# Kernel tuning notes

Measured on AMD Instinct MI355X. Metric: run time of the kernel, lower is better.

The kernel has to match this reference:

```python
import jax, jax.numpy as jnp
import numpy as np

N_NODES = 100000
N_EDGES = 1600000
HIDDEN = 64
EDGE_DIM = 16


def setup_inputs() -> dict:
    key = jax.random.key(0)
    ks = jax.random.split(key, 9)
    x = jax.random.normal(ks[0], (N_NODES, HIDDEN), dtype=jnp.float32)
    edge_index = jax.random.randint(ks[1], (2, N_EDGES), 0, N_NODES, dtype=jnp.int32)
    edge_attr = jax.random.normal(ks[2], (N_EDGES, EDGE_DIM), dtype=jnp.float32)
    s1 = 1.0 / np.sqrt(HIDDEN * 2 + EDGE_DIM)
    s2 = 1.0 / np.sqrt(HIDDEN)
    s3 = 1.0 / np.sqrt(HIDDEN * 2)
    W1 = jax.random.uniform(ks[3], (HIDDEN * 2 + EDGE_DIM, HIDDEN), jnp.float32, -s1, s1)
    b1 = jax.random.uniform(ks[4], (HIDDEN,), jnp.float32, -s1, s1)
    W2 = jax.random.uniform(ks[5], (HIDDEN, HIDDEN), jnp.float32, -s2, s2)
    b2 = jax.random.uniform(ks[6], (HIDDEN,), jnp.float32, -s2, s2)
    W3 = jax.random.uniform(ks[7], (HIDDEN * 2, HIDDEN), jnp.float32, -s3, s3)
    b3 = jax.random.uniform(ks[8], (HIDDEN,), jnp.float32, -s3, s3)
    return {"x": x, "edge_index": edge_index, "edge_attr": edge_attr,
            "W1": W1, "b1": b1, "W2": W2, "b2": b2, "W3": W3, "b3": b3}


def reference(x, edge_index, edge_attr, W1, b1, W2, b2, W3, b3):
    src, dst = edge_index[0], edge_index[1]
    # edge MLP: Linear -> SiLU -> Linear -> SiLU
    m_in = jnp.concatenate([x[src], x[dst], edge_attr], axis=-1)  # [E, 2H+Ed]
    h = jax.nn.silu(m_in @ W1 + b1)
    messages = jax.nn.silu(h @ W2 + b2)  # [E, H]
    # scatter-add aggregate onto destination nodes
    agg = jax.ops.segment_sum(messages, dst, num_segments=x.shape[0])  # [N, H]
    # node MLP: Linear -> SiLU
    node_in = jnp.concatenate([x, agg], axis=-1)  # [N, 2H]
    return jax.nn.silu(node_in @ W3 + b3)
```

## Files before the change

kernel.cpp:

```cpp
#include <hip/hip_runtime.h>
#include <hip/hip_bf16.h>

#define NE 1600000
#define NN 100000
#define H 64
#define ED 16
#define NT (NE / 64)
#define NB1 391
#define NNB 1563

#define KS  72
#define K3S 136
#define YS  68

typedef __attribute__((ext_vector_type(8))) short short8;
typedef __attribute__((ext_vector_type(4))) float floatx4;

__device__ __forceinline__ unsigned short f2bf(float f) {
    union { float f; unsigned u; } v; v.f = f;
    unsigned r = v.u + 0x7fff + ((v.u >> 16) & 1);
    return (unsigned short)(r >> 16);
}

__device__ __forceinline__ float bf2f(unsigned short u) {
    union { unsigned u; float f; } v; v.u = ((unsigned)u) << 16;
    return v.f;
}

__device__ __forceinline__ unsigned cvt_pk_bf16(float lo, float hi) {
    unsigned r;
    asm("v_cvt_pk_bf16_f32 %0, %1, %2" : "=v"(r) : "v"(lo), "v"(hi));
    return r;
}

__device__ __forceinline__ float silu(float x) {
    return x * __builtin_amdgcn_rcpf(1.0f + __expf(-x));
}

__global__ void prep_kernel(const float* __restrict__ x,
                            const float* __restrict__ W1,
                            const float* __restrict__ b1,
                            const float* __restrict__ W2,
                            const float* __restrict__ W3,
                            const int* __restrict__ ei,
                            unsigned short* __restrict__ xb,
                            unsigned short* __restrict__ W1abT,
                            unsigned short* __restrict__ W1cT,
                            unsigned short* __restrict__ W2T,
                            unsigned short* __restrict__ W3T,
                            int* __restrict__ cnt,
                            int* __restrict__ rank,
                            float4* __restrict__ aggv) {
    int tid = blockIdx.x * blockDim.x + threadIdx.x;
    int nt = gridDim.x * blockDim.x;
    const float4* xv = (const float4*)x;
    uint2* xbv = (uint2*)xb;
    for (int i = tid; i < NN * H / 4; i += nt) {
        float4 v = xv[i];
        uint2 o;
        o.x = cvt_pk_bf16(v.x, v.y);
        o.y = cvt_pk_bf16(v.z, v.w);
        xbv[i] = o;
    }
    {
        float4 z = {0.f, 0.f, 0.f, 0.f};
        for (int i = tid; i < NN * H / 4; i += nt) aggv[i] = z;
    }
    for (int i = tid; i < 128 * KS; i += nt) {
        int n = i / KS, k = i % KS;
        W1abT[i] = (k < 64) ? f2bf(W1[(size_t)((n < 64) ? k : 64 + k) * 64 + (n & 63)])
                            : (unsigned short)0;
    }
    for (int i = tid; i < 64 * 32; i += nt) {
        int n = i / 32, k = i % 32;
        unsigned short v = 0;
        if (k < 16) v = f2bf(W1[(size_t)(128 + k) * 64 + n]);
        else if (k == 16) v = f2bf(b1[n]);
        W1cT[i] = v;
    }
    for (int i = tid; i < 64 * KS; i += nt) {
        int n = i / KS, k = i % KS;
        W2T[i] = (k < 64) ? f2bf(W2[k * 64 + n]) : (unsigned short)0;
    }
    for (int i = tid; i < 64 * K3S; i += nt) {
        int n = i / K3S, k = i % K3S;
        W3T[i] = (k < 128) ? f2bf(W3[k * 64 + n]) : (unsigned short)0;
    }
    for (int e = tid; e < NE; e += nt) {
        rank[e] = atomicAdd(&cnt[ei[NE + e]], 1);
    }
}

__global__ void scan_block_kernel(const int* __restrict__ cnt,
                                  int* __restrict__ offs,
                                  int* __restrict__ bsums) {
    __shared__ int tmp[256];
    int b = blockIdx.x, i = threadIdx.x, idx = b * 256 + i;
    int v = (idx < NN) ? cnt[idx] : 0;
    tmp[i] = v;
    __syncthreads();
    #pragma unroll
    for (int off = 1; off < 256; off <<= 1) {
        int t2 = (i >= off) ? tmp[i - off] : 0;
        __syncthreads();
        tmp[i] += t2;
        __syncthreads();
    }
    if (idx < NN) offs[idx] = tmp[i] - v;
    if (i == 255) bsums[b] = tmp[255];
}

__global__ void scan_sums_kernel(int* __restrict__ bsums) {
    __shared__ int tmp[512];
    int i = threadIdx.x;
    int v = (i < NB1) ? bsums[i] : 0;
    tmp[i] = v;
    __syncthreads();
    #pragma unroll
    for (int off = 1; off < 512; off <<= 1) {
        int t2 = (i >= off) ? tmp[i - off] : 0;
        __syncthreads();
        tmp[i] += t2;
        __syncthreads();
    }
    if (i < NB1) bsums[i] = tmp[i] - v;
}

__global__ void scan_add_kernel(int* __restrict__ offs,
                                const int* __restrict__ bsums) {
    int b = blockIdx.x, idx = b * 256 + threadIdx.x;
    if (idx < NN) {
        offs[idx] += bsums[b];
    }
}

__global__ void scatter_kernel(const int* __restrict__ ei,
                               const int* __restrict__ offs,
                               const int* __restrict__ rank,
                               unsigned long long* __restrict__ sSDE) {
    int e = blockIdx.x * 256 + threadIdx.x;
    int src = ei[e], dst = ei[NE + e];
    int pos = offs[dst] + rank[e];
    unsigned long long v = (unsigned long long)src
                         | ((unsigned long long)dst << 17)
                         | ((unsigned long long)e << 34);
    sSDE[pos] = v;
}

__global__ __launch_bounds__(256) void y12_kernel(
    const unsigned short* __restrict__ xb,
    const unsigned short* __restrict__ W1abT,
    unsigned short* __restrict__ yc) {
    __shared__ unsigned short sW[128 * KS];
    int t = threadIdx.x;
    {
        const uint4* wv = (const uint4*)W1abT;
        uint4* sv = (uint4*)sW;
        for (int i = t; i < 128 * KS * 2 / 16; i += 256) sv[i] = wv[i];
    }
    __syncthreads();

    int lane = t & 63, w = t >> 6;
    int m = lane & 15, q = lane >> 4;
    int n0 = blockIdx.x * 64;
    int node = n0 + w * 16 + m;
    int nclamp = (node < NN) ? node : (NN - 1);

    floatx4 acc[8];
    #pragma unroll
    for (int i = 0; i < 8; i++) acc[i] = (floatx4){0.f, 0.f, 0.f, 0.f};
    #pragma unroll
    for (int kt = 0; kt < 2; kt++) {
        short8 bfr = *(const short8*)(xb + (size_t)nclamp * H + kt * 32 + q * 8);
        #pragma unroll
        for (int tt = 0; tt < 8; tt++) {
            short8 afr = *(const short8*)(sW + (tt * 16 + m) * KS + kt * 32 + q * 8);
            acc[tt] = __builtin_amdgcn_mfma_f32_16x16x32_bf16(afr, bfr, acc[tt], 0, 0, 0);
        }
    }
    if (node < NN) {
        #pragma unroll
        for (int tt = 0; tt < 8; tt++) {
            uint2 o;
            o.x = cvt_pk_bf16(acc[tt][0], acc[tt][1]);
            o.y = cvt_pk_bf16(acc[tt][2], acc[tt][3]);
            *(uint2*)(yc + (size_t)node * 128 + tt * 16 + q * 4) = o;
        }
    }
}

__global__ __launch_bounds__(256, 8) void edge_kernel(
    const unsigned short* __restrict__ yc,
    const float* __restrict__ ea,
    const unsigned long long* __restrict__ sSDE,
    const unsigned short* __restrict__ W1cT,
    const unsigned short* __restrict__ W2T,
    const float* __restrict__ b2,
    float* __restrict__ agg) {
    __shared__ float sWS[4][1088];
    __shared__ int sDst[64];

    int t = threadIdx.x;
    int lane = t & 63, w = t >> 6;
    int m = lane & 15, q = lane >> 4;
    int E = w * 16 + m;

    unsigned long long sde = sSDE[(size_t)blockIdx.x * 64 + E];
    int src = (int)(sde & 0x1FFFF);
    int dst = (int)((sde >> 17) & 0x1FFFF);
    int e   = (int)(sde >> 34);
    if (q == 0) sDst[E] = dst;

    union uf { unsigned u[4]; short8 s; };
    uf idA, idB;
    {
        unsigned val = (m & 1) ? 0x3F800000u : 0x00003F80u;
        int wsel = (m >> 1) & 3;
        bool gA = (q == (m >> 3));
        bool gB = (q == 2 + (m >> 3));
        #pragma unroll
        for (int i = 0; i < 4; i++) {
            idA.u[i] = (gA && wsel == i) ? val : 0u;
            idB.u[i] = (gB && wsel == i) ? val : 0u;
        }
    }

    short8 y1f0 = *(const short8*)(yc + (size_t)src * 128 + q * 8);
    short8 y1f1 = *(const short8*)(yc + (size_t)src * 128 + 32 + q * 8);
    short8 y2f0 = *(const short8*)(yc + (size_t)dst * 128 + 64 + q * 8);
    short8 y2f1 = *(const short8*)(yc + (size_t)dst * 128 + 96 + q * 8);

    short8 bf1 = {0, 0, 0, 0, 0, 0, 0, 0};
    if (q < 2) {
        const float4* p = (const float4*)(ea + (size_t)e * ED + q * 8);
        float4 v0 = p[0], v1 = p[1];
        union { unsigned u[4]; short8 s; } ub;
        ub.u[0] = cvt_pk_bf16(v0.x, v0.y);
        ub.u[1] = cvt_pk_bf16(v0.z, v0.w);
        ub.u[2] = cvt_pk_bf16(v1.x, v1.y);
        ub.u[3] = cvt_pk_bf16(v1.z, v1.w);
        bf1 = ub.s;
    } else if (q == 2) {
        bf1[0] = (short)0x3F80;
    }

    floatx4 acc[4];
    #pragma unroll
    for (int tt = 0; tt < 4; tt++) {
        short8 w1c = *(const short8*)(W1cT + (tt * 16 + m) * 32 + q * 8);
        floatx4 a = (floatx4){0.f, 0.f, 0.f, 0.f};
        a = __builtin_amdgcn_mfma_f32_16x16x32_bf16(w1c, bf1, a, 0, 0, 0);
        short8 idt = (tt & 1) ? idB.s : idA.s;
        a = __builtin_amdgcn_mfma_f32_16x16x32_bf16(idt, (tt >> 1) ? y1f1 : y1f0, a, 0, 0, 0);
        a = __builtin_amdgcn_mfma_f32_16x16x32_bf16(idt, (tt >> 1) ? y2f1 : y2f0, a, 0, 0, 0);
        acc[tt] = a;
    }

    unsigned short* sHw = (unsigned short*)sWS[w];
    #pragma unroll
    for (int tt = 0; tt < 4; tt++) {
        uint2 hp;
        hp.x = cvt_pk_bf16(silu(acc[tt][0]), silu(acc[tt][1]));
        hp.y = cvt_pk_bf16(silu(acc[tt][2]), silu(acc[tt][3]));
        *(uint2*)(sHw + m * KS + tt * 16 + q * 4) = hp;
    }

    floatx4 acc2[4];
    #pragma unroll
    for (int i = 0; i < 4; i++) acc2[i] = (floatx4){0.f, 0.f, 0.f, 0.f};
    #pragma unroll
    for (int kt = 0; kt < 2; kt++) {
        short8 hfr = *(const short8*)(sHw + m * KS + kt * 32 + q * 8);
        #pragma unroll
        for (int tt = 0; tt < 4; tt++) {
            short8 w2 = *(const short8*)(W2T + (tt * 16 + m) * KS + kt * 32 + q * 8);
            acc2[tt] = __builtin_amdgcn_mfma_f32_16x16x32_bf16(w2, hfr, acc2[tt], 0, 0, 0);
        }
    }

    float* sMw = sWS[w];
    #pragma unroll
    for (int tt = 0; tt < 4; tt++) {
        float4 bb = *(const float4*)(b2 + tt * 16 + q * 4);
        float4 mv;
        mv.x = silu(acc2[tt][0] + bb.x);
        mv.y = silu(acc2[tt][1] + bb.y);
        mv.z = silu(acc2[tt][2] + bb.z);
        mv.w = silu(acc2[tt][3] + bb.w);
        *(float4*)(sMw + m * YS + tt * 16 + q * 4) = mv;
    }

    {
        int c = lane;
        float s = 0.f;
        int cur = sDst[w * 16];
        #pragma unroll
        for (int r = 0; r < 16; r++) {
            int d = sDst[w * 16 + r];
            if (d != cur) {
                atomicAdd(&agg[(size_t)cur * H + c], s);
                s = 0.f;
                cur = d;
            }
            s += sMw[r * YS + c];
        }
        atomicAdd(&agg[(size_t)cur * H + c], s);
    }
}

__global__ __launch_bounds__(256) void node_kernel(
    const unsigned short* __restrict__ xb,
    const float* __restrict__ agg,
    const unsigned short* __restrict__ W3T,
    const float* __restrict__ b3,
    float* __restrict__ out) {
    __shared__ unsigned short sW3[64 * K3S];
    __shared__ unsigned short sA[64 * K3S];

    int t = threadIdx.x;
    int n0 = blockIdx.x * 64;

    {
        const uint4* wv = (const uint4*)W3T;
        uint4* sv = (uint4*)sW3;
        for (int i = t; i < 64 * K3S * 2 / 16; i += 256) sv[i] = wv[i];
    }
    {
        int nL = t >> 2, sub = t & 3;
        int node = n0 + nL;
        uint4* arow = (uint4*)(sA + nL * K3S);
        if (node < NN) {
            const uint4* xs = (const uint4*)(xb + (size_t)node * H);
            arow[sub * 2]     = xs[sub * 2];
            arow[sub * 2 + 1] = xs[sub * 2 + 1];
            const float4* av = (const float4*)(agg + (size_t)node * H);
            unsigned tmp[8];
            #pragma unroll
            for (int j = 0; j < 4; j++) {
                float4 v = av[sub * 4 + j];
                tmp[j * 2 + 0] = cvt_pk_bf16(v.x, v.y);
                tmp[j * 2 + 1] = cvt_pk_bf16(v.z, v.w);
            }
            uint4* drow = (uint4*)(sA + nL * K3S + 64 + sub * 16);
            drow[0] = ((const uint4*)tmp)[0];
            drow[1] = ((const uint4*)tmp)[1];
        } else {
            uint4 z = {0, 0, 0, 0};
            arow[sub * 2] = z; arow[sub * 2 + 1] = z;
            uint4* drow = (uint4*)(sA + nL * K3S + 64 + sub * 16);
            drow[0] = z; drow[1] = z;
        }
    }
    __syncthreads();

    int w = t >> 6, lane = t & 63;
    int m = lane & 15, q = lane >> 4;
    int node = n0 + w * 16 + m;

    floatx4 acc[4];
    #pragma unroll
    for (int i = 0; i < 4; i++) acc[i] = (floatx4){0.f, 0.f, 0.f, 0.f};
    #pragma unroll
    for (int kt = 0; kt < 4; kt++) {
        short8 bfr = *(const short8*)(sA + (w * 16 + m) * K3S + kt * 32 + q * 8);
        #pragma unroll
        for (int tt = 0; tt < 4; tt++) {
            short8 afr = *(const short8*)(sW3 + (tt * 16 + m) * K3S + kt * 32 + q * 8);
            acc[tt] = __builtin_amdgcn_mfma_f32_16x16x32_bf16(afr, bfr, acc[tt], 0, 0, 0);
        }
    }
    if (node < NN) {
        #pragma unroll
        for (int tt = 0; tt < 4; tt++) {
            float4 bb = *(const float4*)(b3 + tt * 16 + q * 4);
            float4 ov;
            ov.x = silu(acc[tt][0] + bb.x);
            ov.y = silu(acc[tt][1] + bb.y);
            ov.z = silu(acc[tt][2] + bb.z);
            ov.w = silu(acc[tt][3] + bb.w);
            *(float4*)(out + (size_t)node * H + tt * 16 + q * 4) = ov;
        }
    }
}

static inline size_t align256(size_t x) { return (x + 255) & ~(size_t)255; }

extern "C" void kernel_launch(void* const* d_in, const int* in_sizes, int n_in,
                              void* d_out, int out_size, void* d_ws, size_t ws_size,
                              hipStream_t stream) {
    const float* x  = (const float*)d_in[0];
    const int*   ei = (const int*)d_in[1];
    const float* ea = (const float*)d_in[2];
    const float* W1 = (const float*)d_in[3];
    const float* b1 = (const float*)d_in[4];
    const float* W2 = (const float*)d_in[5];
    const float* b2 = (const float*)d_in[6];
    const float* W3 = (const float*)d_in[7];
    const float* b3 = (const float*)d_in[8];
    float* out = (float*)d_out;

    char* ws = (char*)d_ws;
    size_t o = 0;
    float* agg = (float*)(ws + o);                    o = align256(o + (size_t)NN * H * 4);
    unsigned short* xb = (unsigned short*)(ws + o);   o = align256(o + (size_t)NN * H * 2);
    unsigned short* yc = (unsigned short*)(ws + o);   o = align256(o + (size_t)NN * 128 * 2);
    unsigned short* W1abT = (unsigned short*)(ws + o); o = align256(o + 128 * KS * 2);
    unsigned short* W1cT = (unsigned short*)(ws + o); o = align256(o + 64 * 32 * 2);
    unsigned short* W2T = (unsigned short*)(ws + o);  o = align256(o + 64 * KS * 2);
    unsigned short* W3T = (unsigned short*)(ws + o);  o = align256(o + 64 * K3S * 2);
    int* offs = (int*)(ws + o);                       o = align256(o + (size_t)NN * 4);
    int* bsums = (int*)(ws + o);                      o = align256(o + NB1 * 4);
    int* cnt = (int*)(ws + o);                        o = align256(o + (size_t)NN * 4);
    int* rank = (int*)(ws + o);                       o = align256(o + (size_t)NE * 4);
    unsigned long long* sSDE = (unsigned long long*)(ws + o); o = align256(o + (size_t)NE * 8);

    hipMemsetAsync(cnt, 0, (size_t)NN * sizeof(int), stream);
    prep_kernel<<<2048, 256, 0, stream>>>(x, W1, b1, W2, W3, ei, xb, W1abT, W1cT, W2T, W3T,
                                          cnt, rank, (float4*)agg);
    scan_block_kernel<<<NB1, 256, 0, stream>>>(cnt, offs, bsums);
    scan_sums_kernel<<<1, 512, 0, stream>>>(bsums);
    scan_add_kernel<<<NB1, 256, 0, stream>>>(offs, bsums);
    scatter_kernel<<<NE / 256, 256, 0, stream>>>(ei, offs, rank, sSDE);
    y12_kernel<<<NNB, 256, 0, stream>>>(xb, W1abT, yc);
    edge_kernel<<<NT, 256, 0, stream>>>(yc, ea, sSDE, W1cT, W2T, b2, agg);
    node_kernel<<<NNB, 256, 0, stream>>>(xb, agg, W3T, b3, out);
}
```

Baseline: 425.2 us.

## Fuse scan-add, scatter and y12 GEMM into one interleaved launch

Drops the scan_add kernel by adding the block prefix sum inline when computing scatter positions. It also merges the scatter and y12 projection kernels into one grid, with every fifth block doing the node GEMM and the rest doing edge scatter. This removes two launches and their gaps and lets memory-bound scatter overlap with MFMA work. The cost is an extra bsums load per edge, and every block now reserves the GEMM's shared memory, which may lower occupancy for scatter blocks.

```diff
diff --git a/kernel.cpp b/kernel.cpp
--- a/kernel.cpp
+++ b/kernel.cpp
@@ -8,6 +8,8 @@
 #define NT (NE / 64)
 #define NB1 391
 #define NNB 1563
+#define NSB 6250
+#define NFB (NSB + NNB)
 
 #define KS  72
 #define K3S 136
@@ -20,11 +22,6 @@
     union { float f; unsigned u; } v; v.f = f;
     unsigned r = v.u + 0x7fff + ((v.u >> 16) & 1);
     return (unsigned short)(r >> 16);
-}
-
-__device__ __forceinline__ float bf2f(unsigned short u) {
-    union { unsigned u; float f; } v; v.u = ((unsigned)u) << 16;
-    return v.f;
 }
 
 __device__ __forceinline__ unsigned cvt_pk_bf16(float lo, float hi) {
@@ -126,66 +123,63 @@
     if (i < NB1) bsums[i] = tmp[i] - v;
 }
 
-__global__ void scan_add_kernel(int* __restrict__ offs,
-                                const int* __restrict__ bsums) {
-    int b = blockIdx.x, idx = b * 256 + threadIdx.x;
-    if (idx < NN) {
-        offs[idx] += bsums[b];
-    }
-}
-
-__global__ void scatter_kernel(const int* __restrict__ ei,
-                               const int* __restrict__ offs,
-                               const int* __restrict__ rank,
-                               unsigned long long* __restrict__ sSDE) {
-    int e = blockIdx.x * 256 + threadIdx.x;
-    int src = ei[e], dst = ei[NE + e];
-    int pos = offs[dst] + rank[e];
-    unsigned long long v = (unsigned long long)src
-                         | ((unsigned long long)dst << 17)
-                         | ((unsigned long long)e << 34);
-    sSDE[pos] = v;
-}
-
-__global__ __launch_bounds__(256) void y12_kernel(
+__global__ __launch_bounds__(256) void scatter_y12_kernel(
+    const int* __restrict__ ei,
+    const int* __restrict__ offs,
+    const int* __restrict__ bsums,
+    const int* __restrict__ rank,
+    unsigned long long* __restrict__ sSDE,
     const unsigned short* __restrict__ xb,
     const unsigned short* __restrict__ W1abT,
     unsigned short* __restrict__ yc) {
     __shared__ unsigned short sW[128 * KS];
+    int bid = blockIdx.x;
     int t = threadIdx.x;
-    {
-        const uint4* wv = (const uint4*)W1abT;
-        uint4* sv = (uint4*)sW;
-        for (int i = t; i < 128 * KS * 2 / 16; i += 256) sv[i] = wv[i];
-    }
-    __syncthreads();
-
-    int lane = t & 63, w = t >> 6;
-    int m = lane & 15, q = lane >> 4;
-    int n0 = blockIdx.x * 64;
-    int node = n0 + w * 16 + m;
-    int nclamp = (node < NN) ? node : (NN - 1);
-
-    floatx4 acc[8];
-    #pragma unroll
-    for (int i = 0; i < 8; i++) acc[i] = (floatx4){0.f, 0.f, 0.f, 0.f};
-    #pragma unroll
-    for (int kt = 0; kt < 2; kt++) {
-        short8 bfr = *(const short8*)(xb + (size_t)nclamp * H + kt * 32 + q * 8);
-        #pragma unroll
-        for (int tt = 0; tt < 8; tt++) {
-            short8 afr = *(const short8*)(sW + (tt * 16 + m) * KS + kt * 32 + q * 8);
-            acc[tt] = __builtin_amdgcn_mfma_f32_16x16x32_bf16(afr, bfr, acc[tt], 0, 0, 0);
-        }
-    }
-    if (node < NN) {
-        #pragma unroll
-        for (int tt = 0; tt < 8; tt++) {
-            uint2 o;
-            o.x = cvt_pk_bf16(acc[tt][0], acc[tt][1]);
-            o.y = cvt_pk_bf16(acc[tt][2], acc[tt][3]);
-            *(uint2*)(yc + (size_t)node * 128 + tt * 16 + q * 4) = o;
-        }
+
+    if (bid % 5 == 0) {
+        {
+            const uint4* wv = (const uint4*)W1abT;
+            uint4* sv = (uint4*)sW;
+            for (int i = t; i < 128 * KS * 2 / 16; i += 256) sv[i] = wv[i];
+        }
+        __syncthreads();
+
+        int lane = t & 63, w = t >> 6;
+        int m = lane & 15, q = lane >> 4;
+        int n0 = (bid / 5) * 64;
+        int node = n0 + w * 16 + m;
+        int nclamp = (node < NN) ? node : (NN - 1);
+
+        floatx4 acc[8];
+        #pragma unroll
+        for (int i = 0; i < 8; i++) acc[i] = (floatx4){0.f, 0.f, 0.f, 0.f};
+        #pragma unroll
+        for (int kt = 0; kt < 2; kt++) {
+            short8 bfr = *(const short8*)(xb + (size_t)nclamp * H + kt * 32 + q * 8);
+            #pragma unroll
+            for (int tt = 0; tt < 8; tt++) {
+                short8 afr = *(const short8*)(sW + (tt * 16 + m) * KS + kt * 32 + q * 8);
+                acc[tt] = __builtin_amdgcn_mfma_f32_16x16x32_bf16(afr, bfr, acc[tt], 0, 0, 0);
+            }
+        }
+        if (node < NN) {
+            #pragma unroll
+            for (int tt = 0; tt < 8; tt++) {
+                uint2 o;
+                o.x = cvt_pk_bf16(acc[tt][0], acc[tt][1]);
+                o.y = cvt_pk_bf16(acc[tt][2], acc[tt][3]);
+                *(uint2*)(yc + (size_t)node * 128 + tt * 16 + q * 4) = o;
+            }
+        }
+    } else {
+        int sidx = bid - bid / 5 - 1;
+        int e = sidx * 256 + t;
+        int src = ei[e], dst = ei[NE + e];
+        int pos = offs[dst] + bsums[dst >> 8] + rank[e];
+        unsigned long long v = (unsigned long long)src
+                             | ((unsigned long long)dst << 17)
+                             | ((unsigned long long)e << 34);
+        sSDE[pos] = v;
     }
 }
 
@@ -419,9 +413,7 @@
                                           cnt, rank, (float4*)agg);
     scan_block_kernel<<<NB1, 256, 0, stream>>>(cnt, offs, bsums);
     scan_sums_kernel<<<1, 512, 0, stream>>>(bsums);
-    scan_add_kernel<<<NB1, 256, 0, stream>>>(offs, bsums);
-    scatter_kernel<<<NE / 256, 256, 0, stream>>>(ei, offs, rank, sSDE);
-    y12_kernel<<<NNB, 256, 0, stream>>>(xb, W1abT, yc);
+    scatter_y12_kernel<<<NFB, 256, 0, stream>>>(ei, offs, bsums, rank, sSDE, xb, W1abT, yc);
     edge_kernel<<<NT, 256, 0, stream>>>(yc, ea, sSDE, W1cT, W2T, b2, agg);
     node_kernel<<<NNB, 256, 0, stream>>>(xb, agg, W3T, b3, out);
 }
```

Result: no change. 424.1 us (-0.3%).
